# Kernel optimization log

Measured on AMD Instinct MI355X. Metric: run time of the kernel, lower is better.

## Reference

```python
import jax, jax.numpy as jnp
import numpy as np

ENCODE_SIZE = 64
SCALE = (2 * ENCODE_SIZE) ** (-0.5)  # matches torch module: (2*encode_size)^-0.5


def setup_inputs() -> dict:
    key = jax.random.key(0)
    kq, kk, kv = jax.random.split(key, 3)
    B, Lq, Lk, D = 16, 2048, 2048, 128
    return {
        "query": jax.random.normal(kq, (B, Lq, D), dtype=jnp.float32),
        "key": jax.random.normal(kk, (B, Lk, D), dtype=jnp.float32),
        "value": jax.random.normal(kv, (B, Lk, D), dtype=jnp.float32),
    }


def reference(query, key, value):
    # atten = softmax(Q K^T * scale) ; context = atten @ V
    # Dropout is identity in eval mode.
    scores = jnp.einsum("bqd,bkd->bqk", query, key) * SCALE  # [B, Lq, Lk]
    atten = jax.nn.softmax(scores, axis=2)
    context = jnp.einsum("bqk,bkd->bqd", atten, value)  # [B, Lq, D]
    return (context, atten)
```

## Files before the change

### kernel.cpp

```cpp
#include <hip/hip_runtime.h>
#include <hip/hip_bf16.h>

#define B_N   16
#define LL    2048
#define DD    128
#define NW    8
#define QBLK  16
#define KCOLS (LL / NW)
#define NT    (KCOLS / 16)

typedef float f32x4  __attribute__((ext_vector_type(4)));
typedef short bf16x8 __attribute__((ext_vector_type(8)));

__device__ __forceinline__ short f2bf(float x) {
  union { float f; unsigned u; } v; v.f = x;
  unsigned r = (v.u + 0x7FFFu + ((v.u >> 16) & 1u)) >> 16;
  return (short)r;
}
__device__ __forceinline__ float bf2f(short x) {
  union { unsigned u; float f; } v; v.u = ((unsigned)(unsigned short)x) << 16;
  return v.f;
}

__global__ void cvt_qk(const float4* __restrict__ Q, const float4* __restrict__ K,
                       short4* __restrict__ Qb, short4* __restrict__ Kb, int nvec) {
  int stride = gridDim.x * blockDim.x;
  for (int i = blockIdx.x * blockDim.x + threadIdx.x; i < 2 * nvec; i += stride) {
    int sel = (i < nvec);
    int idx = sel ? i : i - nvec;
    float4 v = sel ? Q[idx] : K[idx];
    short4 o;
    o.x = f2bf(v.x); o.y = f2bf(v.y); o.z = f2bf(v.z); o.w = f2bf(v.w);
    if (sel) Qb[idx] = o; else Kb[idx] = o;
  }
}

__global__ void transpose_v(const float* __restrict__ V, short* __restrict__ Vt) {
  __shared__ short t[32][33];
  int b = blockIdx.z, k0 = blockIdx.x * 32, d0 = blockIdx.y * 32;
  int tx = threadIdx.x, ty = threadIdx.y;
#pragma unroll
  for (int i = 0; i < 4; ++i) {
    int k = k0 + ty + i * 8;
    t[ty + i * 8][tx] = f2bf(V[((size_t)b * LL + k) * DD + d0 + tx]);
  }
  __syncthreads();
#pragma unroll
  for (int i = 0; i < 4; ++i) {
    int d = d0 + ty + i * 8;
    Vt[((size_t)b * DD + d) * LL + k0 + tx] = t[tx][ty + i * 8];
  }
}

__global__ __launch_bounds__(512, 4) void attn_fused(
    const short* __restrict__ Qb, const short* __restrict__ Kb,
    const short* __restrict__ Vt, float* __restrict__ ctx,
    float* __restrict__ att) {
  __shared__ short Pl[QBLK * LL];
  __shared__ float redS[NW][QBLK];

  const int tid  = threadIdx.x;
  const int lane = tid & 63;
  const int w    = tid >> 6;
  const int g    = lane >> 4;
  const int lr   = lane & 15;

  const int wg    = ((blockIdx.x & 7) << 8) | (blockIdx.x >> 3);
  const int batch = wg >> 7;
  const int q0    = (wg & 127) * QBLK;

  const bf16x8* qp = (const bf16x8*)(Qb + (size_t)(batch * LL + q0 + lr) * DD);
  bf16x8 qf[4];
#pragma unroll
  for (int kk = 0; kk < 4; ++kk) qf[kk] = qp[kk * 4 + g];

  const int c0w = w * KCOLS;
  const short* kb = Kb + (size_t)(batch * LL + c0w + lr) * DD;

  const float SCALE2 = 0.08838834764831845f * 1.4426950408889634f;

  float rs[4] = {0.f, 0.f, 0.f, 0.f};

  bf16x8 kf[2][4];
#pragma unroll
  for (int kk = 0; kk < 4; ++kk) kf[0][kk] = ((const bf16x8*)kb)[kk * 4 + g];

#pragma unroll
  for (int t = 0; t < NT; ++t) {
    if (t + 1 < NT) {
      const bf16x8* kp = (const bf16x8*)(kb + (t + 1) * 16 * DD);
#pragma unroll
      for (int kk = 0; kk < 4; ++kk) kf[(t + 1) & 1][kk] = kp[kk * 4 + g];
    }
    f32x4 s = (f32x4){0.f, 0.f, 0.f, 0.f};
#pragma unroll
    for (int kk = 0; kk < 4; ++kk)
      s = __builtin_amdgcn_mfma_f32_16x16x32_bf16(qf[kk], kf[t & 1][kk], s, 0, 0, 0);
#pragma unroll
    for (int j = 0; j < 4; ++j) {
      float p = exp2f(s[j] * SCALE2);
      rs[j] += p;
      int r = 4 * g + j;
      Pl[(r * LL + c0w + t * 16 + lr) ^ ((r & 7) << 3)] = f2bf(p);
    }
  }

#pragma unroll
  for (int j = 0; j < 4; ++j) {
    float ss = rs[j];
    ss += __shfl_xor(ss, 1, 16);
    ss += __shfl_xor(ss, 2, 16);
    ss += __shfl_xor(ss, 4, 16);
    ss += __shfl_xor(ss, 8, 16);
    rs[j] = ss;
  }
  if (lr == 0) {
#pragma unroll
    for (int j = 0; j < 4; ++j) redS[w][4 * g + j] = rs[j];
  }
  __syncthreads();

  float rinv[4];
#pragma unroll
  for (int j = 0; j < 4; ++j) {
    float ss = redS[0][4 * g + j];
#pragma unroll
    for (int ww = 1; ww < NW; ++ww) ss += redS[ww][4 * g + j];
    rinv[j] = 1.0f / ss;
  }

  float* attb = att + (size_t)batch * LL * LL;
#pragma unroll
  for (int t = 0; t < NT; ++t) {
#pragma unroll
    for (int j = 0; j < 4; ++j) {
      int r = 4 * g + j;
      int c = c0w + t * 16 + lr;
      float p = bf2f(Pl[(r * LL + c) ^ ((r & 7) << 3)]) * rinv[j];
      attb[(size_t)(q0 + r) * LL + c] = p;
    }
  }

  f32x4 c2 = (f32x4){0.f, 0.f, 0.f, 0.f};
  const bf16x8* vp = (const bf16x8*)(Vt + (size_t)(batch * DD + w * 16 + lr) * LL);
#pragma unroll 8
  for (int kk = 0; kk < LL / 32; ++kk) {
    int ke = kk * 32 + g * 8;
    bf16x8 af = *(const bf16x8*)(Pl + ((lr * LL + ke) ^ ((lr & 7) << 3)));
    c2 = __builtin_amdgcn_mfma_f32_16x16x32_bf16(af, vp[kk * 4 + g], c2, 0, 0, 0);
  }

#pragma unroll
  for (int j = 0; j < 4; ++j)
    ctx[(size_t)(batch * LL + q0 + 4 * g + j) * DD + w * 16 + lr] = c2[j] * rinv[j];
}

extern "C" void kernel_launch(void* const* d_in, const int* in_sizes, int n_in,
                              void* d_out, int out_size, void* d_ws, size_t ws_size,
                              hipStream_t stream) {
  const float* Q = (const float*)d_in[0];
  const float* K = (const float*)d_in[1];
  const float* V = (const float*)d_in[2];

  float* ctx = (float*)d_out;
  float* att = ctx + (size_t)B_N * LL * DD;

  short* Qb = (short*)d_ws;
  short* Kb = Qb + (size_t)B_N * LL * DD;
  short* Vt = Kb + (size_t)B_N * LL * DD;

  const int nvec = B_N * LL * DD / 4;
  cvt_qk<<<2048, 256, 0, stream>>>((const float4*)Q, (const float4*)K,
                                   (short4*)Qb, (short4*)Kb, nvec);
  transpose_v<<<dim3(LL / 32, DD / 32, B_N), dim3(32, 8), 0, stream>>>(V, Vt);
  attn_fused<<<2048, 512, 0, stream>>>(Qb, Kb, Vt, ctx, att);
}
```

Measured before the change: 537.0 us.

## Halve query block to raise occupancy, vectorize attention store and V transpose

The query block shrinks from 16 to 8 rows. This halves the LDS probability buffer to 32KB and lets 8 blocks fit per CU, with twice as many blocks launched. The MFMA still computes 16 rows, so half the lanes' work is wasted. The attention-matrix writeback is reorganized so each wave writes one full row with float4 stores instead of scattered scalar stores. The V transpose uses 64x64 tiles with vectorized loads and stores, and the K register double-buffering is removed.

```diff
diff --git a/kernel.cpp b/kernel.cpp
--- a/kernel.cpp
+++ b/kernel.cpp
@@ -5,12 +5,13 @@
 #define LL    2048
 #define DD    128
 #define NW    8
-#define QBLK  16
+#define QBLK  8
 #define KCOLS (LL / NW)
 #define NT    (KCOLS / 16)
 
-typedef float f32x4  __attribute__((ext_vector_type(4)));
-typedef short bf16x8 __attribute__((ext_vector_type(8)));
+typedef float  f32x4   __attribute__((ext_vector_type(4)));
+typedef short  bf16x8  __attribute__((ext_vector_type(8)));
+typedef short  short4v __attribute__((ext_vector_type(4)));
 
 __device__ __forceinline__ short f2bf(float x) {
   union { float f; unsigned u; } v; v.f = x;
@@ -22,37 +23,52 @@
   return v.f;
 }
 
+#if __has_builtin(__builtin_amdgcn_exp2f)
+#define EXP2(x) __builtin_amdgcn_exp2f(x)
+#else
+#define EXP2(x) exp2f(x)
+#endif
+
 __global__ void cvt_qk(const float4* __restrict__ Q, const float4* __restrict__ K,
-                       short4* __restrict__ Qb, short4* __restrict__ Kb, int nvec) {
+                       short4v* __restrict__ Qb, short4v* __restrict__ Kb, int nvec) {
   int stride = gridDim.x * blockDim.x;
   for (int i = blockIdx.x * blockDim.x + threadIdx.x; i < 2 * nvec; i += stride) {
     int sel = (i < nvec);
     int idx = sel ? i : i - nvec;
     float4 v = sel ? Q[idx] : K[idx];
-    short4 o;
-    o.x = f2bf(v.x); o.y = f2bf(v.y); o.z = f2bf(v.z); o.w = f2bf(v.w);
+    short4v o;
+    o[0] = f2bf(v.x); o[1] = f2bf(v.y); o[2] = f2bf(v.z); o[3] = f2bf(v.w);
     if (sel) Qb[idx] = o; else Kb[idx] = o;
   }
 }
 
+#define TS 64
+#define TSTR 68
 __global__ void transpose_v(const float* __restrict__ V, short* __restrict__ Vt) {
-  __shared__ short t[32][33];
-  int b = blockIdx.z, k0 = blockIdx.x * 32, d0 = blockIdx.y * 32;
-  int tx = threadIdx.x, ty = threadIdx.y;
+  __shared__ short t[TS * TSTR];
+  const int b = blockIdx.z, k0 = blockIdx.x * TS, d0 = blockIdx.y * TS;
+  const int tid = threadIdx.x;
+  const int m = tid & 15, kq = tid >> 4;
 #pragma unroll
-  for (int i = 0; i < 4; ++i) {
-    int k = k0 + ty + i * 8;
-    t[ty + i * 8][tx] = f2bf(V[((size_t)b * LL + k) * DD + d0 + tx]);
+  for (int it = 0; it < 4; ++it) {
+    int k = kq + it * 16;
+    float4 v = *(const float4*)&V[(size_t)(b * LL + k0 + k) * DD + d0 + 4 * m];
+    t[(4 * m + 0) * TSTR + k] = f2bf(v.x);
+    t[(4 * m + 1) * TSTR + k] = f2bf(v.y);
+    t[(4 * m + 2) * TSTR + k] = f2bf(v.z);
+    t[(4 * m + 3) * TSTR + k] = f2bf(v.w);
   }
   __syncthreads();
 #pragma unroll
-  for (int i = 0; i < 4; ++i) {
-    int d = d0 + ty + i * 8;
-    Vt[((size_t)b * DD + d) * LL + k0 + tx] = t[tx][ty + i * 8];
+  for (int it = 0; it < 4; ++it) {
+    int d  = (tid >> 4) + it * 16;
+    int kx = 4 * (tid & 15);
+    short4v o = *(const short4v*)&t[d * TSTR + kx];
+    *(short4v*)&Vt[(size_t)(b * DD + d0 + d) * LL + k0 + kx] = o;
   }
 }
 
-__global__ __launch_bounds__(512, 4) void attn_fused(
+__global__ __launch_bounds__(512, 8) void attn_fused(
     const short* __restrict__ Qb, const short* __restrict__ Kb,
     const short* __restrict__ Vt, float* __restrict__ ctx,
     float* __restrict__ att) {
@@ -65,11 +81,11 @@
   const int g    = lane >> 4;
   const int lr   = lane & 15;
 
-  const int wg    = ((blockIdx.x & 7) << 8) | (blockIdx.x >> 3);
-  const int batch = wg >> 7;
-  const int q0    = (wg & 127) * QBLK;
+  const int wg    = ((blockIdx.x & 7) << 9) | (blockIdx.x >> 3);
+  const int batch = wg >> 8;
+  const int q0    = (wg & 255) * QBLK;
 
-  const bf16x8* qp = (const bf16x8*)(Qb + (size_t)(batch * LL + q0 + lr) * DD);
+  const bf16x8* qp = (const bf16x8*)(Qb + (size_t)(batch * LL + q0 + (lr & 7)) * DD);
   bf16x8 qf[4];
 #pragma unroll
   for (int kk = 0; kk < 4; ++kk) qf[kk] = qp[kk * 4 + g];
@@ -78,30 +94,25 @@
   const short* kb = Kb + (size_t)(batch * LL + c0w + lr) * DD;
 
   const float SCALE2 = 0.08838834764831845f * 1.4426950408889634f;
-
   float rs[4] = {0.f, 0.f, 0.f, 0.f};
-
-  bf16x8 kf[2][4];
-#pragma unroll
-  for (int kk = 0; kk < 4; ++kk) kf[0][kk] = ((const bf16x8*)kb)[kk * 4 + g];
 
 #pragma unroll
   for (int t = 0; t < NT; ++t) {
-    if (t + 1 < NT) {
-      const bf16x8* kp = (const bf16x8*)(kb + (t + 1) * 16 * DD);
+    const bf16x8* kp = (const bf16x8*)(kb + t * 16 * DD);
+    bf16x8 k0f = kp[g], k1f = kp[4 + g], k2f = kp[8 + g], k3f = kp[12 + g];
+    f32x4 s = (f32x4){0.f, 0.f, 0.f, 0.f};
+    s = __builtin_amdgcn_mfma_f32_16x16x32_bf16(qf[0], k0f, s, 0, 0, 0);
+    s = __builtin_amdgcn_mfma_f32_16x16x32_bf16(qf[1], k1f, s, 0, 0, 0);
+    s = __builtin_amdgcn_mfma_f32_16x16x32_bf16(qf[2], k2f, s, 0, 0, 0);
+    s = __builtin_amdgcn_mfma_f32_16x16x32_bf16(qf[3], k3f, s, 0, 0, 0);
+    if (g < 2) {
 #pragma unroll
-      for (int kk = 0; kk < 4; ++kk) kf[(t + 1) & 1][kk] = kp[kk * 4 + g];
-    }
-    f32x4 s = (f32x4){0.f, 0.f, 0.f, 0.f};
-#pragma unroll
-    for (int kk = 0; kk < 4; ++kk)
-      s = __builtin_amdgcn_mfma_f32_16x16x32_bf16(qf[kk], kf[t & 1][kk], s, 0, 0, 0);
-#pragma unroll
-    for (int j = 0; j < 4; ++j) {
-      float p = exp2f(s[j] * SCALE2);
-      rs[j] += p;
-      int r = 4 * g + j;
-      Pl[(r * LL + c0w + t * 16 + lr) ^ ((r & 7) << 3)] = f2bf(p);
+      for (int j = 0; j < 4; ++j) {
+        float p = EXP2(s[j] * SCALE2);
+        rs[j] += p;
+        int r = 4 * g + j;
+        Pl[(r * LL + c0w + t * 16 + lr) ^ (r << 3)] = f2bf(p);
+      }
     }
   }
 
@@ -114,45 +125,53 @@
     ss += __shfl_xor(ss, 8, 16);
     rs[j] = ss;
   }
-  if (lr == 0) {
+  if (lr == 0 && g < 2) {
 #pragma unroll
     for (int j = 0; j < 4; ++j) redS[w][4 * g + j] = rs[j];
   }
   __syncthreads();
 
-  float rinv[4];
+  float rsum = 0.f;
 #pragma unroll
-  for (int j = 0; j < 4; ++j) {
-    float ss = redS[0][4 * g + j];
+  for (int ww = 0; ww < NW; ++ww) rsum += redS[ww][w];
+  const float rinvw = 1.0f / rsum;
+  float* attrow = att + (size_t)batch * LL * LL + (size_t)(q0 + w) * LL;
 #pragma unroll
-    for (int ww = 1; ww < NW; ++ww) ss += redS[ww][4 * g + j];
-    rinv[j] = 1.0f / ss;
+  for (int v = 0; v < 8; ++v) {
+    int c0 = v * 256 + lane * 4;
+    short4v p4 = *(const short4v*)(Pl + ((w * LL + c0) ^ (w << 3)));
+    float4 o;
+    o.x = bf2f(p4[0]) * rinvw;
+    o.y = bf2f(p4[1]) * rinvw;
+    o.z = bf2f(p4[2]) * rinvw;
+    o.w = bf2f(p4[3]) * rinvw;
+    *(float4*)(attrow + c0) = o;
   }
 
-  float* attb = att + (size_t)batch * LL * LL;
-#pragma unroll
-  for (int t = 0; t < NT; ++t) {
+  float rinv[4];
+  if (g < 2) {
 #pragma unroll
     for (int j = 0; j < 4; ++j) {
-      int r = 4 * g + j;
-      int c = c0w + t * 16 + lr;
-      float p = bf2f(Pl[(r * LL + c) ^ ((r & 7) << 3)]) * rinv[j];
-      attb[(size_t)(q0 + r) * LL + c] = p;
+      float ss = 0.f;
+#pragma unroll
+      for (int ww = 0; ww < NW; ++ww) ss += redS[ww][4 * g + j];
+      rinv[j] = 1.0f / ss;
     }
   }
 
   f32x4 c2 = (f32x4){0.f, 0.f, 0.f, 0.f};
   const bf16x8* vp = (const bf16x8*)(Vt + (size_t)(batch * DD + w * 16 + lr) * LL);
+  const int pr = lr & 7;
 #pragma unroll 8
   for (int kk = 0; kk < LL / 32; ++kk) {
-    int ke = kk * 32 + g * 8;
-    bf16x8 af = *(const bf16x8*)(Pl + ((lr * LL + ke) ^ ((lr & 7) << 3)));
+    bf16x8 af = *(const bf16x8*)(Pl + ((pr * LL + kk * 32 + g * 8) ^ (pr << 3)));
     c2 = __builtin_amdgcn_mfma_f32_16x16x32_bf16(af, vp[kk * 4 + g], c2, 0, 0, 0);
   }
-
+  if (g < 2) {
 #pragma unroll
-  for (int j = 0; j < 4; ++j)
-    ctx[(size_t)(batch * LL + q0 + 4 * g + j) * DD + w * 16 + lr] = c2[j] * rinv[j];
+    for (int j = 0; j < 4; ++j)
+      ctx[(size_t)(batch * LL + q0 + 4 * g + j) * DD + w * 16 + lr] = c2[j] * rinv[j];
+  }
 }
 
 extern "C" void kernel_launch(void* const* d_in, const int* in_sizes, int n_in,
@@ -171,7 +190,7 @@
 
   const int nvec = B_N * LL * DD / 4;
   cvt_qk<<<2048, 256, 0, stream>>>((const float4*)Q, (const float4*)K,
-                                   (short4*)Qb, (short4*)Kb, nvec);
-  transpose_v<<<dim3(LL / 32, DD / 32, B_N), dim3(32, 8), 0, stream>>>(V, Vt);
-  attn_fused<<<2048, 512, 0, stream>>>(Qb, Kb, Vt, ctx, att);
+                                   (short4v*)Qb, (short4v*)Kb, nvec);
+  transpose_v<<<dim3(LL / TS, DD / TS, B_N), 256, 0, stream>>>(V, Vt);
+  attn_fused<<<4096, 512, 0, stream>>>(Qb, Kb, Vt, ctx, att);
 }
```

After: 745.0 us. +38.7%, slower.
